# Kernel tuning notes

Hardware: AMD Instinct MI355X
Metric: run time of the kernel (lower is better)

The kernel has to match this reference:

```python
import jax, jax.numpy as jnp
import numpy as np

BOUND = 1.0
MIN_NEAR = 0.05
NUM_STEPS = 64
UP_STEPS = 64
DENSITY_SCALE = 1.0
N_RAYS = 16384
HIDDEN = 64


def setup_inputs() -> dict:
    key = jax.random.key(0)
    ks = jax.random.split(key, 8)
    # cameras hover near z=2 looking roughly toward -z so rays hit the [-1,1]^3 AABB
    rays_o = jax.random.normal(ks[0], (N_RAYS, 3), jnp.float32) * 0.1 + jnp.array([0.0, 0.0, 2.0])
    rays_d = jax.random.normal(ks[1], (N_RAYS, 3), jnp.float32) * 0.2 + jnp.array([0.0, 0.0, -1.0])
    rays_d = rays_d / jnp.linalg.norm(rays_d, axis=-1, keepdims=True)
    W1 = jax.random.normal(ks[2], (3, HIDDEN), jnp.float32) / jnp.sqrt(3.0)
    b1 = jnp.zeros((HIDDEN,), jnp.float32)
    w_sigma = jax.random.normal(ks[3], (HIDDEN, 1), jnp.float32) / jnp.sqrt(float(HIDDEN))
    b_sigma = jnp.zeros((1,), jnp.float32)
    W_rgb = jax.random.normal(ks[4], (HIDDEN, 3), jnp.float32) / jnp.sqrt(float(HIDDEN))
    b_rgb = jnp.zeros((3,), jnp.float32)
    return {"rays_o": rays_o, "rays_d": rays_d, "W1": W1, "b1": b1,
            "w_sigma": w_sigma, "b_sigma": b_sigma, "W_rgb": W_rgb, "b_rgb": b_rgb}


def near_far_cube(rays_o, rays_d, bound, min_near):
    tmin = (-bound - rays_o) / (rays_d + 1e-15)
    tmax = (bound - rays_o) / (rays_d + 1e-15)
    near = jnp.max(jnp.minimum(tmin, tmax), axis=-1, keepdims=True)
    far = jnp.min(jnp.maximum(tmin, tmax), axis=-1, keepdims=True)
    miss = far < near
    near = jnp.where(miss, 1e9, near)
    far = jnp.where(miss, 1e9, far)
    near = jnp.maximum(near, min_near)
    return near, far


def sample_pdf(bins, weights, n_samples):
    # bins: [N, M+1], weights: [N, M]; deterministic (det=True) inverse-CDF sampling
    weights = weights + 1e-5
    pdf = weights / jnp.sum(weights, -1, keepdims=True)
    cdf = jnp.cumsum(pdf, -1)
    cdf = jnp.concatenate([jnp.zeros_like(cdf[..., :1]), cdf], -1)  # [N, M+1]
    u = jnp.linspace(0.5 / n_samples, 1.0 - 0.5 / n_samples, n_samples, dtype=cdf.dtype)
    u = jnp.broadcast_to(u, cdf.shape[:-1] + (n_samples,))
    inds = jax.vmap(lambda c, uu: jnp.searchsorted(c, uu, side='right'))(cdf, u)
    below = jnp.maximum(inds - 1, 0)
    above = jnp.minimum(inds, cdf.shape[-1] - 1)
    cdf_b = jnp.take_along_axis(cdf, below, -1)
    cdf_a = jnp.take_along_axis(cdf, above, -1)
    bins_b = jnp.take_along_axis(bins, below, -1)
    bins_a = jnp.take_along_axis(bins, above, -1)
    denom = cdf_a - cdf_b
    denom = jnp.where(denom < 1e-5, jnp.ones_like(denom), denom)
    t = (u - cdf_b) / denom
    return bins_b + t * (bins_a - bins_b)


def mlp(pts, W1, b1, w_sigma, b_sigma, W_rgb, b_rgb):
    h = jax.nn.relu(pts @ W1 + b1)                      # [N, T, HIDDEN]
    sigma = jax.nn.softplus(h @ w_sigma + b_sigma)[..., 0]  # [N, T]
    rgb = jax.nn.sigmoid(h @ W_rgb + b_rgb)             # [N, T, 3]
    return sigma, rgb


def alpha_composite_weights(z_vals, sigma, sample_dist):
    deltas = z_vals[..., 1:] - z_vals[..., :-1]
    deltas = jnp.concatenate([deltas, jnp.broadcast_to(sample_dist, deltas[..., :1].shape)], -1)
    alphas = 1.0 - jnp.exp(-deltas * DENSITY_SCALE * sigma)
    trans = jnp.cumprod(jnp.concatenate([jnp.ones_like(alphas[..., :1]), 1.0 - alphas + 1e-15], -1)[..., :-1], -1)
    return alphas * trans


def reference(rays_o, rays_d, W1, b1, w_sigma, b_sigma, W_rgb, b_rgb):
    rays_d = rays_d / jnp.linalg.norm(rays_d, axis=-1, keepdims=True)
    near, far = near_far_cube(rays_o, rays_d, BOUND, MIN_NEAR)  # [N,1]
    sample_dist = (far - near) / NUM_STEPS                      # [N,1]

    # coarse stratified (deterministic) samples
    z = jnp.linspace(0.0, 1.0, NUM_STEPS, dtype=rays_o.dtype)
    z_vals = near + (far - near) * z                            # [N,T]
    xyzs = rays_o[:, None, :] + rays_d[:, None, :] * z_vals[..., None]
    xyzs = jnp.clip(xyzs, -BOUND, BOUND)
    sigma, _ = mlp(xyzs, W1, b1, w_sigma, b_sigma, W_rgb, b_rgb)
    weights = alpha_composite_weights(z_vals, sigma, sample_dist)

    # inverse-CDF importance resampling (no-grad in original)
    z_mid = 0.5 * (z_vals[..., :-1] + z_vals[..., 1:])          # [N,T-1]
    new_z = sample_pdf(z_mid, weights[:, 1:-1], UP_STEPS)       # [N,UP]
    new_z = jax.lax.stop_gradient(new_z)

    z_all = jnp.sort(jnp.concatenate([z_vals, new_z], -1), -1)  # [N,T+UP]
    xyzs_all = rays_o[:, None, :] + rays_d[:, None, :] * z_all[..., None]
    xyzs_all = jnp.clip(xyzs_all, -BOUND, BOUND)
    sigma_all, rgb_all = mlp(xyzs_all, W1, b1, w_sigma, b_sigma, W_rgb, b_rgb)
    weights_all = alpha_composite_weights(z_all, sigma_all, sample_dist)

    weights_sum = jnp.sum(weights_all, -1)                      # [N]
    image = jnp.sum(weights_all[..., None] * rgb_all, axis=-2)  # [N,3]
    image = image + (1.0 - weights_sum)[..., None]              # white background
    return image
```

## Files before the change

kernel.cpp:

```cpp
#include <hip/hip_runtime.h>
#include <math.h>

#define WAVES_PER_BLOCK 4

typedef float v2f __attribute__((ext_vector_type(2)));
typedef float v4f __attribute__((ext_vector_type(4)));

__device__ __forceinline__ v2f v2_fma(v2f a, v2f b, v2f c) {
    return __builtin_elementwise_fma(a, b, c);
}
__device__ __forceinline__ v2f v2_max0(v2f a) {
    return __builtin_elementwise_max(a, (v2f){0.0f, 0.0f});
}
__device__ __forceinline__ v2f v2_splat(float x) { return (v2f){x, x}; }

__device__ __forceinline__ float fast_rcp(float x) { return __builtin_amdgcn_rcpf(x); }

#define DPP_ROW_SHR(n)  (0x110 | (n))
#define DPP_WF_SL1      0x130
#define DPP_WF_SR1      0x138
#define DPP_ROW_BCAST15 0x142
#define DPP_ROW_BCAST31 0x143

template <int CTRL, int RM = 0xf, int BM = 0xf, bool BC = false>
__device__ __forceinline__ float fdpp(float old_, float src) {
    return __int_as_float(__builtin_amdgcn_update_dpp(
        __float_as_int(old_), __float_as_int(src), CTRL, RM, BM, BC));
}

__device__ __forceinline__ float lane63_bcast(float x) {
    return __int_as_float(__builtin_amdgcn_readlane(__float_as_int(x), 63));
}
__device__ __forceinline__ float rdlane(float x, int l) {
    return __int_as_float(__builtin_amdgcn_readlane(__float_as_int(x), l));
}

__device__ __forceinline__ float scan_add_dpp(float x) {
    x += fdpp<DPP_ROW_SHR(1)>(0.0f, x);
    x += fdpp<DPP_ROW_SHR(2)>(0.0f, x);
    x += fdpp<DPP_ROW_SHR(4)>(0.0f, x);
    x += fdpp<DPP_ROW_SHR(8)>(0.0f, x);
    x += fdpp<DPP_ROW_BCAST15, 0xa>(0.0f, x);
    x += fdpp<DPP_ROW_BCAST31, 0xc>(0.0f, x);
    return x;
}
__device__ __forceinline__ float scan_mul_dpp(float x) {
    x *= fdpp<DPP_ROW_SHR(1)>(1.0f, x);
    x *= fdpp<DPP_ROW_SHR(2)>(1.0f, x);
    x *= fdpp<DPP_ROW_SHR(4)>(1.0f, x);
    x *= fdpp<DPP_ROW_SHR(8)>(1.0f, x);
    x *= fdpp<DPP_ROW_BCAST15, 0xa>(1.0f, x);
    x *= fdpp<DPP_ROW_BCAST31, 0xc>(1.0f, x);
    return x;
}
__device__ __forceinline__ float wave_sum_dpp(float x) {
    return lane63_bcast(scan_add_dpp(x));
}

__device__ __forceinline__ float softplus_f(float x) {
    return fmaxf(x, 0.0f) + __logf(1.0f + __expf(-fabsf(x)));
}
__device__ __forceinline__ float sigmoid_f(float x) {
    return fast_rcp(1.0f + __expf(-x));
}
__device__ __forceinline__ float clamp1(float x) {
    return fminf(fmaxf(x, -1.0f), 1.0f);
}

template <bool LE>
__device__ __forceinline__ int rank2(const float* a, float own, float x) {
    int o = 0;
#pragma unroll
    for (int t = 0; t < 8; ++t) {
        float p = rdlane(own, 8 * t + 7);
        o += (int)(LE ? (p <= x) : (p < x));
    }
    o = (o < 7) ? o : 7;
    const v4f q0 = *(const v4f*)&a[8 * o];
    const v4f q1 = *(const v4f*)&a[8 * o + 4];
    int cnt = 0;
    cnt += (int)(LE ? (q0.x <= x) : (q0.x < x));
    cnt += (int)(LE ? (q0.y <= x) : (q0.y < x));
    cnt += (int)(LE ? (q0.z <= x) : (q0.z < x));
    cnt += (int)(LE ? (q0.w <= x) : (q0.w < x));
    cnt += (int)(LE ? (q1.x <= x) : (q1.x < x));
    cnt += (int)(LE ? (q1.y <= x) : (q1.y < x));
    cnt += (int)(LE ? (q1.z <= x) : (q1.z < x));
    cnt += (int)(LE ? (q1.w <= x) : (q1.w < x));
    return 8 * o + cnt;
}

__global__ __launch_bounds__(WAVES_PER_BLOCK * 64)
void nerf_render_kernel(const float* __restrict__ rays_o,
                        const float* __restrict__ rays_d,
                        const float* __restrict__ W1,
                        const float* __restrict__ b1,
                        const float* __restrict__ w_sigma,
                        const float* __restrict__ b_sigma,
                        const float* __restrict__ W_rgb,
                        const float* __restrict__ b_rgb,
                        float* __restrict__ out)
{
    const int tid  = threadIdx.x;
    const int lane = tid & 63;
    const int wv   = tid >> 6;
    const int ray  = __builtin_amdgcn_readfirstlane(blockIdx.x * WAVES_PER_BLOCK + wv);

    __shared__ __align__(16) float s_cm  [WAVES_PER_BLOCK][128];
    __shared__ __align__(16) float s_zmid[WAVES_PER_BLOCK][64];
    __shared__ __align__(16) float s_cdf [WAVES_PER_BLOCK][64];
    __shared__ __align__(16) float s_zall[WAVES_PER_BLOCK][128];

    float ox = rays_o[ray * 3 + 0], oy = rays_o[ray * 3 + 1], oz = rays_o[ray * 3 + 2];
    float dx = rays_d[ray * 3 + 0], dy = rays_d[ray * 3 + 1], dz = rays_d[ray * 3 + 2];
    {
        float inv = __builtin_amdgcn_rsqf(dx * dx + dy * dy + dz * dz);
        dx *= inv; dy *= inv; dz *= inv;
    }

    float rx = fast_rcp(dx + 1e-15f);
    float ry = fast_rcp(dy + 1e-15f);
    float rz = fast_rcp(dz + 1e-15f);
    float t0x = (-1.0f - ox) * rx, t1x = (1.0f - ox) * rx;
    float t0y = (-1.0f - oy) * ry, t1y = (1.0f - oy) * ry;
    float t0z = (-1.0f - oz) * rz, t1z = (1.0f - oz) * rz;
    float nearv = fmaxf(fmaxf(fminf(t0x, t1x), fminf(t0y, t1y)), fminf(t0z, t1z));
    float farv  = fminf(fminf(fmaxf(t0x, t1x), fmaxf(t0y, t1y)), fmaxf(t0z, t1z));
    const bool miss = (farv < nearv);
    if (miss) { nearv = 1e9f; farv = 1e9f; }
    nearv = fmaxf(nearv, 0.05f);
    const float sample_dist = (farv - nearv) * (1.0f / 64.0f);

    const float bs0 = b_sigma[0];
    const float br0 = b_rgb[0], br1 = b_rgb[1], br2 = b_rgb[2];

    {
        float w1x = W1[lane], w1y = W1[64 + lane], w1z = W1[128 + lane];
        float eox = ox, eoy = oy, eoz = oz, msc = 1.0f;
        if (miss) {
            eox = clamp1(fmaf(dx, 1e9f, ox));
            eoy = clamp1(fmaf(dy, 1e9f, oy));
            eoz = clamp1(fmaf(dz, 1e9f, oz));
            msc = 0.0f;
        }
        float cj = fmaf(eox, w1x, fmaf(eoy, w1y, fmaf(eoz, w1z, b1[lane])));
        float mj = msc * fmaf(dx, w1x, fmaf(dy, w1y, dz * w1z));
        int g = (lane >> 1) * 4 + (lane & 1);
        s_cm[wv][g]     = cj;
        s_cm[wv][g + 2] = mj;
    }

    float z = nearv + (farv - nearv) * ((float)lane * (1.0f / 63.0f));

    const v2f* ws2 = (const v2f*)w_sigma;
    v2f z2 = v2_splat(z);
    v2f acc = (v2f){bs0, 0.0f};
#pragma unroll 8
    for (int t = 0; t < 32; ++t) {
        v4f g = *(const v4f*)&s_cm[wv][4 * t];
        v2f h = v2_max0(v2_fma((v2f){g.z, g.w}, z2, (v2f){g.x, g.y}));
        acc = v2_fma(h, ws2[t], acc);
    }
    float sigma = softplus_f(acc.x + acc.y);

    float z_next = fdpp<DPP_WF_SL1>(0.0f, z);
    float delta  = (lane < 63) ? (z_next - z) : sample_dist;
    float alpha  = 1.0f - __expf(-delta * sigma);
    float v      = 1.0f - alpha + 1e-15f;
    float incl   = scan_mul_dpp(v);
    float trans  = fdpp<DPP_WF_SR1>(1.0f, incl);
    float w = alpha * trans;

    float wgt = (lane >= 1 && lane <= 62) ? (w + 1e-5f) : 0.0f;
    float cumw = scan_add_dpp(wgt);
    float total = lane63_bcast(cumw);
    float cdf_incl = cumw * fast_rcp(total);

    float zmid = 0.5f * (z + z_next);
    float cdfv = (lane < 63) ? cdf_incl : 2.0f;
    s_zmid[wv][lane] = (lane < 63) ? zmid : 0.0f;
    s_cdf [wv][lane] = cdfv;

    float u = 0.0078125f + (float)lane * 0.015625f;
    int ind = rank2<true>(s_cdf[wv], cdfv, u);
    int below = ind - 1;
    int above = (ind < 62) ? ind : 62;
    float cb = s_cdf[wv][below], ca = s_cdf[wv][above];
    float bb = s_zmid[wv][below], ba = s_zmid[wv][above];
    float denom = ca - cb;
    if (denom < 1e-5f) denom = 1.0f;
    float t = (u - cb) * fast_rcp(denom);
    float nz = fmaf(t, ba - bb, bb);

    s_zmid[wv][lane] = z;
    s_cdf [wv][lane] = nz;
    int pa = lane + rank2<false>(s_cdf [wv], nz, z);
    int pb = lane + rank2<true >(s_zmid[wv], z,  nz);
    s_zall[wv][pa] = z;
    s_zall[wv][pb] = nz;

    v2f za = *(const v2f*)&s_zall[wv][2 * lane];
    float za0 = za.x;
    float za1 = za.y;

    v2f zz = (v2f){za0, za1};
    v2f s2 = v2_splat(bs0);
    v2f r2 = v2_splat(br0), g2 = v2_splat(br1), bch2 = v2_splat(br2);
#pragma unroll 8
    for (int t = 0; t < 32; ++t) {
        v4f g = *(const v4f*)&s_cm[wv][4 * t];
        int j0 = 2 * t, j1 = 2 * t + 1;
        v2f h0 = v2_max0(v2_fma(v2_splat(g.z), zz, v2_splat(g.x)));
        s2   = v2_fma(h0, v2_splat(w_sigma[j0]),       s2);
        r2   = v2_fma(h0, v2_splat(W_rgb[3 * j0 + 0]), r2);
        g2   = v2_fma(h0, v2_splat(W_rgb[3 * j0 + 1]), g2);
        bch2 = v2_fma(h0, v2_splat(W_rgb[3 * j0 + 2]), bch2);
        v2f h1 = v2_max0(v2_fma(v2_splat(g.w), zz, v2_splat(g.y)));
        s2   = v2_fma(h1, v2_splat(w_sigma[j1]),       s2);
        r2   = v2_fma(h1, v2_splat(W_rgb[3 * j1 + 0]), r2);
        g2   = v2_fma(h1, v2_splat(W_rgb[3 * j1 + 1]), g2);
        bch2 = v2_fma(h1, v2_splat(W_rgb[3 * j1 + 2]), bch2);
    }
    float sg0 = softplus_f(s2.x), sg1 = softplus_f(s2.y);
    float r0 = sigmoid_f(r2.x),   r1 = sigmoid_f(r2.y);
    float g0 = sigmoid_f(g2.x),   g1 = sigmoid_f(g2.y);
    float bl0 = sigmoid_f(bch2.x), bl1 = sigmoid_f(bch2.y);

    float zn0 = fdpp<DPP_WF_SL1>(0.0f, za0);
    float d0 = za1 - za0;
    float d1 = (lane < 63) ? (zn0 - za1) : sample_dist;
    float a0 = 1.0f - __expf(-d0 * sg0);
    float a1 = 1.0f - __expf(-d1 * sg1);
    float v0 = 1.0f - a0 + 1e-15f;
    float v1 = 1.0f - a1 + 1e-15f;
    float local = v0 * v1;
    float incl2 = scan_mul_dpp(local);
    float eprod = fdpp<DPP_WF_SR1>(1.0f, incl2);
    float w0 = a0 * eprod;
    float w1 = a1 * (eprod * v0);

    float wsum = wave_sum_dpp(w0 + w1);
    float rs   = wave_sum_dpp(fmaf(w0, r0,  w1 * r1));
    float gs   = wave_sum_dpp(fmaf(w0, g0,  w1 * g1));
    float bs   = wave_sum_dpp(fmaf(w0, bl0, w1 * bl1));

    if (lane == 0) {
        float bg = 1.0f - wsum;
        out[ray * 3 + 0] = rs + bg;
        out[ray * 3 + 1] = gs + bg;
        out[ray * 3 + 2] = bs + bg;
    }
}

extern "C" void kernel_launch(void* const* d_in, const int* in_sizes, int n_in,
                              void* d_out, int out_size, void* d_ws, size_t ws_size,
                              hipStream_t stream) {
    const float* rays_o  = (const float*)d_in[0];
    const float* rays_d  = (const float*)d_in[1];
    const float* W1      = (const float*)d_in[2];
    const float* b1      = (const float*)d_in[3];
    const float* w_sigma = (const float*)d_in[4];
    const float* b_sigma = (const float*)d_in[5];
    const float* W_rgb   = (const float*)d_in[6];
    const float* b_rgb   = (const float*)d_in[7];
    float* out = (float*)d_out;

    const int n_rays = in_sizes[0] / 3;
    dim3 grid((n_rays + WAVES_PER_BLOCK - 1) / WAVES_PER_BLOCK);
    dim3 block(WAVES_PER_BLOCK * 64);
    hipLaunchKernelGGL(nerf_render_kernel, grid, block, 0, stream,
                       rays_o, rays_d, W1, b1, w_sigma, b_sigma, W_rgb, b_rgb, out);
}
```

Measured before the change: 95.99 us.

## Process two rays per wavefront to share weight loads and add ILP

Each wavefront now renders two rays instead of one. The MLP loops interleave both rays so each weight load and scalar broadcast serves two evaluations, and the two independent FMA chains give the scheduler more instruction-level parallelism. The grid is halved to match. In exchange, register and LDS use per wave roughly double, which may lower occupancy, and the scans and searches for the two rays still run one after the other.

```diff
diff --git a/kernel.cpp b/kernel.cpp
--- a/kernel.cpp
+++ b/kernel.cpp
@@ -2,6 +2,7 @@
 #include <math.h>
 
 #define WAVES_PER_BLOCK 4
+#define RAYS_PER_WAVE 2
 
 typedef float v2f __attribute__((ext_vector_type(2)));
 typedef float v4f __attribute__((ext_vector_type(4)));
@@ -104,151 +105,192 @@
     const int tid  = threadIdx.x;
     const int lane = tid & 63;
     const int wv   = tid >> 6;
-    const int ray  = __builtin_amdgcn_readfirstlane(blockIdx.x * WAVES_PER_BLOCK + wv);
-
-    __shared__ __align__(16) float s_cm  [WAVES_PER_BLOCK][128];
-    __shared__ __align__(16) float s_zmid[WAVES_PER_BLOCK][64];
-    __shared__ __align__(16) float s_cdf [WAVES_PER_BLOCK][64];
-    __shared__ __align__(16) float s_zall[WAVES_PER_BLOCK][128];
-
-    float ox = rays_o[ray * 3 + 0], oy = rays_o[ray * 3 + 1], oz = rays_o[ray * 3 + 2];
-    float dx = rays_d[ray * 3 + 0], dy = rays_d[ray * 3 + 1], dz = rays_d[ray * 3 + 2];
-    {
-        float inv = __builtin_amdgcn_rsqf(dx * dx + dy * dy + dz * dz);
-        dx *= inv; dy *= inv; dz *= inv;
-    }
-
-    float rx = fast_rcp(dx + 1e-15f);
-    float ry = fast_rcp(dy + 1e-15f);
-    float rz = fast_rcp(dz + 1e-15f);
-    float t0x = (-1.0f - ox) * rx, t1x = (1.0f - ox) * rx;
-    float t0y = (-1.0f - oy) * ry, t1y = (1.0f - oy) * ry;
-    float t0z = (-1.0f - oz) * rz, t1z = (1.0f - oz) * rz;
-    float nearv = fmaxf(fmaxf(fminf(t0x, t1x), fminf(t0y, t1y)), fminf(t0z, t1z));
-    float farv  = fminf(fminf(fmaxf(t0x, t1x), fmaxf(t0y, t1y)), fmaxf(t0z, t1z));
-    const bool miss = (farv < nearv);
-    if (miss) { nearv = 1e9f; farv = 1e9f; }
-    nearv = fmaxf(nearv, 0.05f);
-    const float sample_dist = (farv - nearv) * (1.0f / 64.0f);
+    const int ray0 = __builtin_amdgcn_readfirstlane(
+        (blockIdx.x * WAVES_PER_BLOCK + wv) * RAYS_PER_WAVE);
+
+    __shared__ __align__(16) float s_cm  [WAVES_PER_BLOCK][RAYS_PER_WAVE * 128];
+    __shared__ __align__(16) float s_zmid[WAVES_PER_BLOCK][RAYS_PER_WAVE * 64];
+    __shared__ __align__(16) float s_cdf [WAVES_PER_BLOCK][RAYS_PER_WAVE * 64];
+    __shared__ __align__(16) float s_zall[WAVES_PER_BLOCK][RAYS_PER_WAVE * 128];
 
     const float bs0 = b_sigma[0];
     const float br0 = b_rgb[0], br1 = b_rgb[1], br2 = b_rgb[2];
 
-    {
-        float w1x = W1[lane], w1y = W1[64 + lane], w1z = W1[128 + lane];
-        float eox = ox, eoy = oy, eoz = oz, msc = 1.0f;
-        if (miss) {
-            eox = clamp1(fmaf(dx, 1e9f, ox));
-            eoy = clamp1(fmaf(dy, 1e9f, oy));
-            eoz = clamp1(fmaf(dz, 1e9f, oz));
-            msc = 0.0f;
+    float sample_dist[RAYS_PER_WAVE];
+    float zc[RAYS_PER_WAVE];
+
+#pragma unroll
+    for (int r = 0; r < RAYS_PER_WAVE; ++r) {
+        const int ray = ray0 + r;
+        float ox = rays_o[ray * 3 + 0], oy = rays_o[ray * 3 + 1], oz = rays_o[ray * 3 + 2];
+        float dx = rays_d[ray * 3 + 0], dy = rays_d[ray * 3 + 1], dz = rays_d[ray * 3 + 2];
+        {
+            float inv = __builtin_amdgcn_rsqf(dx * dx + dy * dy + dz * dz);
+            dx *= inv; dy *= inv; dz *= inv;
         }
-        float cj = fmaf(eox, w1x, fmaf(eoy, w1y, fmaf(eoz, w1z, b1[lane])));
-        float mj = msc * fmaf(dx, w1x, fmaf(dy, w1y, dz * w1z));
-        int g = (lane >> 1) * 4 + (lane & 1);
-        s_cm[wv][g]     = cj;
-        s_cm[wv][g + 2] = mj;
-    }
-
-    float z = nearv + (farv - nearv) * ((float)lane * (1.0f / 63.0f));
+        float rx = fast_rcp(dx + 1e-15f);
+        float ry = fast_rcp(dy + 1e-15f);
+        float rz = fast_rcp(dz + 1e-15f);
+        float t0x = (-1.0f - ox) * rx, t1x = (1.0f - ox) * rx;
+        float t0y = (-1.0f - oy) * ry, t1y = (1.0f - oy) * ry;
+        float t0z = (-1.0f - oz) * rz, t1z = (1.0f - oz) * rz;
+        float nearv = fmaxf(fmaxf(fminf(t0x, t1x), fminf(t0y, t1y)), fminf(t0z, t1z));
+        float farv  = fminf(fminf(fmaxf(t0x, t1x), fmaxf(t0y, t1y)), fmaxf(t0z, t1z));
+        const bool miss = (farv < nearv);
+        if (miss) { nearv = 1e9f; farv = 1e9f; }
+        nearv = fmaxf(nearv, 0.05f);
+        sample_dist[r] = (farv - nearv) * (1.0f / 64.0f);
+
+        {
+            float w1x = W1[lane], w1y = W1[64 + lane], w1z = W1[128 + lane];
+            float eox = ox, eoy = oy, eoz = oz, msc = 1.0f;
+            if (miss) {
+                eox = clamp1(fmaf(dx, 1e9f, ox));
+                eoy = clamp1(fmaf(dy, 1e9f, oy));
+                eoz = clamp1(fmaf(dz, 1e9f, oz));
+                msc = 0.0f;
+            }
+            float cj = fmaf(eox, w1x, fmaf(eoy, w1y, fmaf(eoz, w1z, b1[lane])));
+            float mj = msc * fmaf(dx, w1x, fmaf(dy, w1y, dz * w1z));
+            int g = (lane >> 1) * 4 + (lane & 1);
+            s_cm[wv][128 * r + g]     = cj;
+            s_cm[wv][128 * r + g + 2] = mj;
+        }
+        zc[r] = nearv + (farv - nearv) * ((float)lane * (1.0f / 63.0f));
+    }
 
     const v2f* ws2 = (const v2f*)w_sigma;
-    v2f z2 = v2_splat(z);
-    v2f acc = (v2f){bs0, 0.0f};
-#pragma unroll 8
+    v2f z2a = v2_splat(zc[0]), z2b = v2_splat(zc[1]);
+    v2f accA = (v2f){bs0, 0.0f}, accB = (v2f){bs0, 0.0f};
+#pragma unroll 4
     for (int t = 0; t < 32; ++t) {
-        v4f g = *(const v4f*)&s_cm[wv][4 * t];
-        v2f h = v2_max0(v2_fma((v2f){g.z, g.w}, z2, (v2f){g.x, g.y}));
-        acc = v2_fma(h, ws2[t], acc);
-    }
-    float sigma = softplus_f(acc.x + acc.y);
-
-    float z_next = fdpp<DPP_WF_SL1>(0.0f, z);
-    float delta  = (lane < 63) ? (z_next - z) : sample_dist;
-    float alpha  = 1.0f - __expf(-delta * sigma);
-    float v      = 1.0f - alpha + 1e-15f;
-    float incl   = scan_mul_dpp(v);
-    float trans  = fdpp<DPP_WF_SR1>(1.0f, incl);
-    float w = alpha * trans;
-
-    float wgt = (lane >= 1 && lane <= 62) ? (w + 1e-5f) : 0.0f;
-    float cumw = scan_add_dpp(wgt);
-    float total = lane63_bcast(cumw);
-    float cdf_incl = cumw * fast_rcp(total);
-
-    float zmid = 0.5f * (z + z_next);
-    float cdfv = (lane < 63) ? cdf_incl : 2.0f;
-    s_zmid[wv][lane] = (lane < 63) ? zmid : 0.0f;
-    s_cdf [wv][lane] = cdfv;
-
-    float u = 0.0078125f + (float)lane * 0.015625f;
-    int ind = rank2<true>(s_cdf[wv], cdfv, u);
-    int below = ind - 1;
-    int above = (ind < 62) ? ind : 62;
-    float cb = s_cdf[wv][below], ca = s_cdf[wv][above];
-    float bb = s_zmid[wv][below], ba = s_zmid[wv][above];
-    float denom = ca - cb;
-    if (denom < 1e-5f) denom = 1.0f;
-    float t = (u - cb) * fast_rcp(denom);
-    float nz = fmaf(t, ba - bb, bb);
-
-    s_zmid[wv][lane] = z;
-    s_cdf [wv][lane] = nz;
-    int pa = lane + rank2<false>(s_cdf [wv], nz, z);
-    int pb = lane + rank2<true >(s_zmid[wv], z,  nz);
-    s_zall[wv][pa] = z;
-    s_zall[wv][pb] = nz;
-
-    v2f za = *(const v2f*)&s_zall[wv][2 * lane];
-    float za0 = za.x;
-    float za1 = za.y;
-
-    v2f zz = (v2f){za0, za1};
-    v2f s2 = v2_splat(bs0);
-    v2f r2 = v2_splat(br0), g2 = v2_splat(br1), bch2 = v2_splat(br2);
-#pragma unroll 8
+        v2f wst = ws2[t];
+        v4f ga = *(const v4f*)&s_cm[wv][4 * t];
+        v4f gb = *(const v4f*)&s_cm[wv][128 + 4 * t];
+        v2f ha = v2_max0(v2_fma((v2f){ga.z, ga.w}, z2a, (v2f){ga.x, ga.y}));
+        v2f hb = v2_max0(v2_fma((v2f){gb.z, gb.w}, z2b, (v2f){gb.x, gb.y}));
+        accA = v2_fma(ha, wst, accA);
+        accB = v2_fma(hb, wst, accB);
+    }
+    float sigma[RAYS_PER_WAVE] = { softplus_f(accA.x + accA.y),
+                                   softplus_f(accB.x + accB.y) };
+
+    float nz[RAYS_PER_WAVE], zn[RAYS_PER_WAVE];
+#pragma unroll
+    for (int r = 0; r < RAYS_PER_WAVE; ++r) {
+        zn[r] = fdpp<DPP_WF_SL1>(0.0f, zc[r]);
+        float delta = (lane < 63) ? (zn[r] - zc[r]) : sample_dist[r];
+        float alpha = 1.0f - __expf(-delta * sigma[r]);
+        float v     = 1.0f - alpha + 1e-15f;
+        float incl  = scan_mul_dpp(v);
+        float trans = fdpp<DPP_WF_SR1>(1.0f, incl);
+        float w = alpha * trans;
+
+        float wgt = (lane >= 1 && lane <= 62) ? (w + 1e-5f) : 0.0f;
+        float cumw = scan_add_dpp(wgt);
+        float total = lane63_bcast(cumw);
+        float cdf_incl = cumw * fast_rcp(total);
+
+        float* zmR  = &s_zmid[wv][64 * r];
+        float* cdfR = &s_cdf [wv][64 * r];
+        float cdfv = (lane < 63) ? cdf_incl : 2.0f;
+        zmR [lane] = (lane < 63) ? (0.5f * (zc[r] + zn[r])) : 0.0f;
+        cdfR[lane] = cdfv;
+
+        float u = 0.0078125f + (float)lane * 0.015625f;
+        int ind = rank2<true>(cdfR, cdfv, u);
+        int below = ind - 1;
+        int above = (ind < 62) ? ind : 62;
+        float cb = cdfR[below], ca = cdfR[above];
+        float bb = zmR [below], ba = zmR [above];
+        float denom = ca - cb;
+        if (denom < 1e-5f) denom = 1.0f;
+        float t = (u - cb) * fast_rcp(denom);
+        nz[r] = fmaf(t, ba - bb, bb);
+    }
+
+    v2f za[RAYS_PER_WAVE];
+#pragma unroll
+    for (int r = 0; r < RAYS_PER_WAVE; ++r) {
+        float* zmR  = &s_zmid[wv][64 * r];
+        float* cdfR = &s_cdf [wv][64 * r];
+        float* zaR  = &s_zall[wv][128 * r];
+        zmR [lane] = zc[r];
+        cdfR[lane] = nz[r];
+        int pa = lane + rank2<false>(cdfR, nz[r], zc[r]);
+        int pb = lane + rank2<true >(zmR,  zc[r], nz[r]);
+        zaR[pa] = zc[r];
+        zaR[pb] = nz[r];
+    }
+#pragma unroll
+    for (int r = 0; r < RAYS_PER_WAVE; ++r)
+        za[r] = *(const v2f*)&s_zall[wv][128 * r + 2 * lane];
+
+    v2f zzA = za[0], zzB = za[1];
+    v2f sA = v2_splat(bs0), rA = v2_splat(br0), gA = v2_splat(br1), bA = v2_splat(br2);
+    v2f sB = v2_splat(bs0), rB = v2_splat(br0), gB = v2_splat(br1), bB = v2_splat(br2);
+#pragma unroll 4
     for (int t = 0; t < 32; ++t) {
-        v4f g = *(const v4f*)&s_cm[wv][4 * t];
         int j0 = 2 * t, j1 = 2 * t + 1;
-        v2f h0 = v2_max0(v2_fma(v2_splat(g.z), zz, v2_splat(g.x)));
-        s2   = v2_fma(h0, v2_splat(w_sigma[j0]),       s2);
-        r2   = v2_fma(h0, v2_splat(W_rgb[3 * j0 + 0]), r2);
-        g2   = v2_fma(h0, v2_splat(W_rgb[3 * j0 + 1]), g2);
-        bch2 = v2_fma(h0, v2_splat(W_rgb[3 * j0 + 2]), bch2);
-        v2f h1 = v2_max0(v2_fma(v2_splat(g.w), zz, v2_splat(g.y)));
-        s2   = v2_fma(h1, v2_splat(w_sigma[j1]),       s2);
-        r2   = v2_fma(h1, v2_splat(W_rgb[3 * j1 + 0]), r2);
-        g2   = v2_fma(h1, v2_splat(W_rgb[3 * j1 + 1]), g2);
-        bch2 = v2_fma(h1, v2_splat(W_rgb[3 * j1 + 2]), bch2);
-    }
-    float sg0 = softplus_f(s2.x), sg1 = softplus_f(s2.y);
-    float r0 = sigmoid_f(r2.x),   r1 = sigmoid_f(r2.y);
-    float g0 = sigmoid_f(g2.x),   g1 = sigmoid_f(g2.y);
-    float bl0 = sigmoid_f(bch2.x), bl1 = sigmoid_f(bch2.y);
-
-    float zn0 = fdpp<DPP_WF_SL1>(0.0f, za0);
-    float d0 = za1 - za0;
-    float d1 = (lane < 63) ? (zn0 - za1) : sample_dist;
-    float a0 = 1.0f - __expf(-d0 * sg0);
-    float a1 = 1.0f - __expf(-d1 * sg1);
-    float v0 = 1.0f - a0 + 1e-15f;
-    float v1 = 1.0f - a1 + 1e-15f;
-    float local = v0 * v1;
-    float incl2 = scan_mul_dpp(local);
-    float eprod = fdpp<DPP_WF_SR1>(1.0f, incl2);
-    float w0 = a0 * eprod;
-    float w1 = a1 * (eprod * v0);
-
-    float wsum = wave_sum_dpp(w0 + w1);
-    float rs   = wave_sum_dpp(fmaf(w0, r0,  w1 * r1));
-    float gs   = wave_sum_dpp(fmaf(w0, g0,  w1 * g1));
-    float bs   = wave_sum_dpp(fmaf(w0, bl0, w1 * bl1));
-
-    if (lane == 0) {
-        float bg = 1.0f - wsum;
-        out[ray * 3 + 0] = rs + bg;
-        out[ray * 3 + 1] = gs + bg;
-        out[ray * 3 + 2] = bs + bg;
+        float ws0 = w_sigma[j0], ws1 = w_sigma[j1];
+        float wr0 = W_rgb[3 * j0 + 0], wg0 = W_rgb[3 * j0 + 1], wb0 = W_rgb[3 * j0 + 2];
+        float wr1 = W_rgb[3 * j1 + 0], wg1 = W_rgb[3 * j1 + 1], wb1 = W_rgb[3 * j1 + 2];
+        v4f ga = *(const v4f*)&s_cm[wv][4 * t];
+        v4f gb = *(const v4f*)&s_cm[wv][128 + 4 * t];
+
+        v2f hA0 = v2_max0(v2_fma(v2_splat(ga.z), zzA, v2_splat(ga.x)));
+        v2f hB0 = v2_max0(v2_fma(v2_splat(gb.z), zzB, v2_splat(gb.x)));
+        sA = v2_fma(hA0, v2_splat(ws0), sA);  sB = v2_fma(hB0, v2_splat(ws0), sB);
+        rA = v2_fma(hA0, v2_splat(wr0), rA);  rB = v2_fma(hB0, v2_splat(wr0), rB);
+        gA = v2_fma(hA0, v2_splat(wg0), gA);  gB = v2_fma(hB0, v2_splat(wg0), gB);
+        bA = v2_fma(hA0, v2_splat(wb0), bA);  bB = v2_fma(hB0, v2_splat(wb0), bB);
+
+        v2f hA1 = v2_max0(v2_fma(v2_splat(ga.w), zzA, v2_splat(ga.y)));
+        v2f hB1 = v2_max0(v2_fma(v2_splat(gb.w), zzB, v2_splat(gb.y)));
+        sA = v2_fma(hA1, v2_splat(ws1), sA);  sB = v2_fma(hB1, v2_splat(ws1), sB);
+        rA = v2_fma(hA1, v2_splat(wr1), rA);  rB = v2_fma(hB1, v2_splat(wr1), rB);
+        gA = v2_fma(hA1, v2_splat(wg1), gA);  gB = v2_fma(hB1, v2_splat(wg1), gB);
+        bA = v2_fma(hA1, v2_splat(wb1), bA);  bB = v2_fma(hB1, v2_splat(wb1), bB);
+    }
+
+#pragma unroll
+    for (int r = 0; r < RAYS_PER_WAVE; ++r) {
+        v2f s2v = (r == 0) ? sA : sB;
+        v2f r2v = (r == 0) ? rA : rB;
+        v2f g2v = (r == 0) ? gA : gB;
+        v2f b2v = (r == 0) ? bA : bB;
+        float za0 = za[r].x, za1 = za[r].y;
+
+        float sg0 = softplus_f(s2v.x), sg1 = softplus_f(s2v.y);
+        float r0 = sigmoid_f(r2v.x),   r1 = sigmoid_f(r2v.y);
+        float g0 = sigmoid_f(g2v.x),   g1 = sigmoid_f(g2v.y);
+        float bl0 = sigmoid_f(b2v.x),  bl1 = sigmoid_f(b2v.y);
+
+        float zn0 = fdpp<DPP_WF_SL1>(0.0f, za0);
+        float d0 = za1 - za0;
+        float d1 = (lane < 63) ? (zn0 - za1) : sample_dist[r];
+        float a0 = 1.0f - __expf(-d0 * sg0);
+        float a1 = 1.0f - __expf(-d1 * sg1);
+        float v0 = 1.0f - a0 + 1e-15f;
+        float v1 = 1.0f - a1 + 1e-15f;
+        float local = v0 * v1;
+        float incl2 = scan_mul_dpp(local);
+        float eprod = fdpp<DPP_WF_SR1>(1.0f, incl2);
+        float w0 = a0 * eprod;
+        float w1 = a1 * (eprod * v0);
+
+        float wsum = wave_sum_dpp(w0 + w1);
+        float rs   = wave_sum_dpp(fmaf(w0, r0,  w1 * r1));
+        float gs   = wave_sum_dpp(fmaf(w0, g0,  w1 * g1));
+        float bs   = wave_sum_dpp(fmaf(w0, bl0, w1 * bl1));
+
+        if (lane == r) {
+            float bg = 1.0f - wsum;
+            const int ray = ray0 + r;
+            out[ray * 3 + 0] = rs + bg;
+            out[ray * 3 + 1] = gs + bg;
+            out[ray * 3 + 2] = bs + bg;
+        }
     }
 }
 
@@ -266,7 +308,8 @@
     float* out = (float*)d_out;
 
     const int n_rays = in_sizes[0] / 3;
-    dim3 grid((n_rays + WAVES_PER_BLOCK - 1) / WAVES_PER_BLOCK);
+    const int rays_per_block = WAVES_PER_BLOCK * RAYS_PER_WAVE;
+    dim3 grid((n_rays + rays_per_block - 1) / rays_per_block);
     dim3 block(WAVES_PER_BLOCK * 64);
     hipLaunchKernelGGL(nerf_render_kernel, grid, block, 0, stream,
                        rays_o, rays_d, W1, b1, w_sigma, b_sigma, W_rgb, b_rgb, out);
```

After: 96.83 us. About the same (+0.9%).

## Replace per-sample MLP loops with piecewise-linear knee prefix sums

Applied to the files above, without the earlier changes.

Each hidden unit along the ray is ReLU(c + m*z), so the network's pre-activations are piecewise linear in z with a breakpoint at -c/m. The kernel sorts those 64 knees, builds prefix sums of the slope and offset contributions for sigma and RGB in shared memory, and evaluates each sample with a rank search plus a few FMAs. This replaces the 64-unit dot-product loops in both MLP passes. It adds setup cost (a rank sort, eight DPP scans, eight wave reductions) and extra shared memory per wave, and floating-point results may differ slightly from the direct sum.

```diff
diff --git a/kernel.cpp b/kernel.cpp
--- a/kernel.cpp
+++ b/kernel.cpp
@@ -5,14 +5,6 @@
 
 typedef float v2f __attribute__((ext_vector_type(2)));
 typedef float v4f __attribute__((ext_vector_type(4)));
-
-__device__ __forceinline__ v2f v2_fma(v2f a, v2f b, v2f c) {
-    return __builtin_elementwise_fma(a, b, c);
-}
-__device__ __forceinline__ v2f v2_max0(v2f a) {
-    return __builtin_elementwise_max(a, (v2f){0.0f, 0.0f});
-}
-__device__ __forceinline__ v2f v2_splat(float x) { return (v2f){x, x}; }
 
 __device__ __forceinline__ float fast_rcp(float x) { return __builtin_amdgcn_rcpf(x); }
 
@@ -106,7 +98,8 @@
     const int wv   = tid >> 6;
     const int ray  = __builtin_amdgcn_readfirstlane(blockIdx.x * WAVES_PER_BLOCK + wv);
 
-    __shared__ __align__(16) float s_cm  [WAVES_PER_BLOCK][128];
+    __shared__ __align__(16) float s_pref[WAVES_PER_BLOCK][65][8];
+    __shared__ __align__(16) float s_kne [WAVES_PER_BLOCK][64];
     __shared__ __align__(16) float s_zmid[WAVES_PER_BLOCK][64];
     __shared__ __align__(16) float s_cdf [WAVES_PER_BLOCK][64];
     __shared__ __align__(16) float s_zall[WAVES_PER_BLOCK][128];
@@ -131,9 +124,12 @@
     nearv = fmaxf(nearv, 0.05f);
     const float sample_dist = (farv - nearv) * (1.0f / 64.0f);
 
-    const float bs0 = b_sigma[0];
-    const float br0 = b_rgb[0], br1 = b_rgb[1], br2 = b_rgb[2];
-
+    const float wS = w_sigma[lane];
+    const float wR = W_rgb[3 * lane + 0];
+    const float wG = W_rgb[3 * lane + 1];
+    const float wB = W_rgb[3 * lane + 2];
+
+    float cj, mj;
     {
         float w1x = W1[lane], w1y = W1[64 + lane], w1z = W1[128 + lane];
         float eox = ox, eoy = oy, eoz = oz, msc = 1.0f;
@@ -143,25 +139,82 @@
             eoz = clamp1(fmaf(dz, 1e9f, oz));
             msc = 0.0f;
         }
-        float cj = fmaf(eox, w1x, fmaf(eoy, w1y, fmaf(eoz, w1z, b1[lane])));
-        float mj = msc * fmaf(dx, w1x, fmaf(dy, w1y, dz * w1z));
-        int g = (lane >> 1) * 4 + (lane & 1);
-        s_cm[wv][g]     = cj;
-        s_cm[wv][g + 2] = mj;
-    }
+        cj = fmaf(eox, w1x, fmaf(eoy, w1y, fmaf(eoz, w1z, b1[lane])));
+        mj = msc * fmaf(dx, w1x, fmaf(dy, w1y, dz * w1z));
+    }
+
+    const bool m0 = (mj == 0.0f);
+    float knee = m0 ? 3e38f : (-cj * fast_rcp(mj));
+    float sgn  = (mj > 0.0f) ? 1.0f : -1.0f;
+    float hm   = 0.5f * fabsf(mj);
+    float hk   = m0 ? 0.0f : (-0.5f * cj * sgn);
+    float pb   = m0 ? fmaxf(cj, 0.0f) : (0.5f * cj);
+    float qb   = 0.5f * mj;
+
+    float gS = wS * hm, gR = wR * hm, gG = wG * hm, gB = wB * hm;
+    float kS = wS * hk, kR = wR * hk, kG = wG * hk, kB = wB * hk;
+
+    float* kneeU = s_zmid[wv];
+    float* kneeS = s_kne[wv];
+    kneeU[lane] = knee;
+    {
+        v4f z4 = (v4f){0.0f, 0.0f, 0.0f, 0.0f};
+        *(v4f*)&s_pref[wv][lane][0] = z4;
+        *(v4f*)&s_pref[wv][lane][4] = z4;
+    }
+    int p = 0;
+#pragma unroll
+    for (int g = 0; g < 16; ++g) {
+        v4f q = *(const v4f*)&kneeU[4 * g];
+        int j = 4 * g;
+        p += (int)((q.x < knee) || ((q.x == knee) && (j + 0 < lane)));
+        p += (int)((q.y < knee) || ((q.y == knee) && (j + 1 < lane)));
+        p += (int)((q.z < knee) || ((q.z == knee) && (j + 2 < lane)));
+        p += (int)((q.w < knee) || ((q.w == knee) && (j + 3 < lane)));
+    }
+    kneeS[p] = knee;
+    *(v4f*)&s_pref[wv][p][0] = (v4f){gS, kS, gR, kR};
+    *(v4f*)&s_pref[wv][p][4] = (v4f){gG, kG, gB, kB};
+
+    v4f d0 = *(const v4f*)&s_pref[wv][lane][0];
+    v4f d1 = *(const v4f*)&s_pref[wv][lane][4];
+    float own_knee = kneeS[lane];
+
+    float iGs = scan_add_dpp(d0.x), iKs = scan_add_dpp(d0.y);
+    float iGr = scan_add_dpp(d0.z), iKr = scan_add_dpp(d0.w);
+    float iGg = scan_add_dpp(d1.x), iKg = scan_add_dpp(d1.y);
+    float iGb = scan_add_dpp(d1.z), iKb = scan_add_dpp(d1.w);
+    float GtS = lane63_bcast(iGs), KtS = lane63_bcast(iKs);
+    float GtR = lane63_bcast(iGr), KtR = lane63_bcast(iKr);
+    float GtG = lane63_bcast(iGg), KtG = lane63_bcast(iKg);
+    float GtB = lane63_bcast(iGb), KtB = lane63_bcast(iKb);
+
+    *(v4f*)&s_pref[wv][lane + 1][0] = (v4f){iGs, iKs, iGr, iKr};
+    *(v4f*)&s_pref[wv][lane + 1][4] = (v4f){iGg, iKg, iGb, iKb};
+    if (lane == 0) {
+        v4f z4 = (v4f){0.0f, 0.0f, 0.0f, 0.0f};
+        *(v4f*)&s_pref[wv][0][0] = z4;
+        *(v4f*)&s_pref[wv][0][4] = z4;
+    }
+
+    float PS = wave_sum_dpp(wS * pb), QS = wave_sum_dpp(wS * qb);
+    float PR = wave_sum_dpp(wR * pb), QR = wave_sum_dpp(wR * qb);
+    float PG = wave_sum_dpp(wG * pb), QG = wave_sum_dpp(wG * qb);
+    float PB = wave_sum_dpp(wB * pb), QB = wave_sum_dpp(wB * qb);
+    const float bs0 = b_sigma[0];
+    const float PpS = PS + KtS + bs0,      QpS = QS - GtS;
+    const float PpR = PR + KtR + b_rgb[0], QpR = QR - GtR;
+    const float PpG = PG + KtG + b_rgb[1], QpG = QG - GtG;
+    const float PpB = PB + KtB + b_rgb[2], QpB = QB - GtB;
 
     float z = nearv + (farv - nearv) * ((float)lane * (1.0f / 63.0f));
-
-    const v2f* ws2 = (const v2f*)w_sigma;
-    v2f z2 = v2_splat(z);
-    v2f acc = (v2f){bs0, 0.0f};
-#pragma unroll 8
-    for (int t = 0; t < 32; ++t) {
-        v4f g = *(const v4f*)&s_cm[wv][4 * t];
-        v2f h = v2_max0(v2_fma((v2f){g.z, g.w}, z2, (v2f){g.x, g.y}));
-        acc = v2_fma(h, ws2[t], acc);
-    }
-    float sigma = softplus_f(acc.x + acc.y);
+    float sigma;
+    {
+        int k = rank2<false>(kneeS, own_knee, z);
+        v2f pk = *(const v2f*)&s_pref[wv][k][0];
+        float pre = fmaf(2.0f, fmaf(pk.x, z, -pk.y), fmaf(QpS, z, PpS));
+        sigma = softplus_f(pre);
+    }
 
     float z_next = fdpp<DPP_WF_SL1>(0.0f, z);
     float delta  = (lane < 63) ? (z_next - z) : sample_dist;
@@ -194,43 +247,41 @@
 
     s_zmid[wv][lane] = z;
     s_cdf [wv][lane] = nz;
-    int pa = lane + rank2<false>(s_cdf [wv], nz, z);
-    int pb = lane + rank2<true >(s_zmid[wv], z,  nz);
-    s_zall[wv][pa] = z;
-    s_zall[wv][pb] = nz;
+    int pa  = lane + rank2<false>(s_cdf [wv], nz, z);
+    int pb2 = lane + rank2<true >(s_zmid[wv], z,  nz);
+    s_zall[wv][pa]  = z;
+    s_zall[wv][pb2] = nz;
 
     v2f za = *(const v2f*)&s_zall[wv][2 * lane];
     float za0 = za.x;
     float za1 = za.y;
 
-    v2f zz = (v2f){za0, za1};
-    v2f s2 = v2_splat(bs0);
-    v2f r2 = v2_splat(br0), g2 = v2_splat(br1), bch2 = v2_splat(br2);
-#pragma unroll 8
-    for (int t = 0; t < 32; ++t) {
-        v4f g = *(const v4f*)&s_cm[wv][4 * t];
-        int j0 = 2 * t, j1 = 2 * t + 1;
-        v2f h0 = v2_max0(v2_fma(v2_splat(g.z), zz, v2_splat(g.x)));
-        s2   = v2_fma(h0, v2_splat(w_sigma[j0]),       s2);
-        r2   = v2_fma(h0, v2_splat(W_rgb[3 * j0 + 0]), r2);
-        g2   = v2_fma(h0, v2_splat(W_rgb[3 * j0 + 1]), g2);
-        bch2 = v2_fma(h0, v2_splat(W_rgb[3 * j0 + 2]), bch2);
-        v2f h1 = v2_max0(v2_fma(v2_splat(g.w), zz, v2_splat(g.y)));
-        s2   = v2_fma(h1, v2_splat(w_sigma[j1]),       s2);
-        r2   = v2_fma(h1, v2_splat(W_rgb[3 * j1 + 0]), r2);
-        g2   = v2_fma(h1, v2_splat(W_rgb[3 * j1 + 1]), g2);
-        bch2 = v2_fma(h1, v2_splat(W_rgb[3 * j1 + 2]), bch2);
-    }
-    float sg0 = softplus_f(s2.x), sg1 = softplus_f(s2.y);
-    float r0 = sigmoid_f(r2.x),   r1 = sigmoid_f(r2.y);
-    float g0 = sigmoid_f(g2.x),   g1 = sigmoid_f(g2.y);
-    float bl0 = sigmoid_f(bch2.x), bl1 = sigmoid_f(bch2.y);
+    int k0 = rank2<false>(kneeS, own_knee, za0);
+    int k1 = rank2<false>(kneeS, own_knee, za1);
+    v4f A0 = *(const v4f*)&s_pref[wv][k0][0];
+    v4f A1 = *(const v4f*)&s_pref[wv][k0][4];
+    v4f B0 = *(const v4f*)&s_pref[wv][k1][0];
+    v4f B1 = *(const v4f*)&s_pref[wv][k1][4];
+
+    float pS0 = fmaf(2.0f, fmaf(A0.x, za0, -A0.y), fmaf(QpS, za0, PpS));
+    float pR0 = fmaf(2.0f, fmaf(A0.z, za0, -A0.w), fmaf(QpR, za0, PpR));
+    float pG0 = fmaf(2.0f, fmaf(A1.x, za0, -A1.y), fmaf(QpG, za0, PpG));
+    float pB0 = fmaf(2.0f, fmaf(A1.z, za0, -A1.w), fmaf(QpB, za0, PpB));
+    float pS1 = fmaf(2.0f, fmaf(B0.x, za1, -B0.y), fmaf(QpS, za1, PpS));
+    float pR1 = fmaf(2.0f, fmaf(B0.z, za1, -B0.w), fmaf(QpR, za1, PpR));
+    float pG1 = fmaf(2.0f, fmaf(B1.x, za1, -B1.y), fmaf(QpG, za1, PpG));
+    float pB1 = fmaf(2.0f, fmaf(B1.z, za1, -B1.w), fmaf(QpB, za1, PpB));
+
+    float sg0 = softplus_f(pS0), sg1 = softplus_f(pS1);
+    float r0 = sigmoid_f(pR0),   r1 = sigmoid_f(pR1);
+    float g0 = sigmoid_f(pG0),   g1 = sigmoid_f(pG1);
+    float bl0 = sigmoid_f(pB0),  bl1 = sigmoid_f(pB1);
 
     float zn0 = fdpp<DPP_WF_SL1>(0.0f, za0);
-    float d0 = za1 - za0;
-    float d1 = (lane < 63) ? (zn0 - za1) : sample_dist;
-    float a0 = 1.0f - __expf(-d0 * sg0);
-    float a1 = 1.0f - __expf(-d1 * sg1);
+    float d0f = za1 - za0;
+    float d1f = (lane < 63) ? (zn0 - za1) : sample_dist;
+    float a0 = 1.0f - __expf(-d0f * sg0);
+    float a1 = 1.0f - __expf(-d1f * sg1);
     float v0 = 1.0f - a0 + 1e-15f;
     float v1 = 1.0f - a1 + 1e-15f;
     float local = v0 * v1;
```

New measurement: 94.09 us. 2.0% less time.
